# Kernel optimization log

Hardware: AMD Instinct MI355X
Metric: run time of the kernel (lower is better)

Reference implementation:

```python
import jax, jax.numpy as jnp
import numpy as np

KROT = 8        # number of pairwise-rotation layers (hard-coded in Rotation)
GROUP = 128     # rotation group size (hard-coded)
QGS = 128       # quantization group size (hard-coded in RotateLinearAWQMarlinInt4)


def setup_inputs() -> dict:
    rng = np.random.default_rng(0)
    M, K, N = 32, 8192, 28672
    G = K // QGS  # 64 quant groups
    shifts = np.arange(8, dtype=np.uint32) * 4
    # activations
    x = jnp.asarray(rng.standard_normal((M, K)), dtype=jnp.float16)
    # int4 weights packed 8-per-int32 along the out dim (nibble j of word n -> column n*8+j)
    nib = rng.integers(0, 16, size=(K, N // 8, 8), dtype=np.uint32)
    qweight = jnp.asarray((nib << shifts).sum(-1, dtype=np.uint32).view(np.int32))  # (K, N//8)
    znib = rng.integers(0, 16, size=(G, N // 8, 8), dtype=np.uint32)
    qzeros = jnp.asarray((znib << shifts).sum(-1, dtype=np.uint32).view(np.int32))  # (G, N//8)
    scales = jnp.asarray(rng.uniform(0.001, 0.01, (G, N)), dtype=jnp.float16)
    bias = jnp.asarray(rng.standard_normal(N) * 0.01, dtype=jnp.float16)
    # rotation params: per-layer angles over all K//2 pairs; one local permutation of
    # 0..127 per layer, shared across all K//GROUP groups (as in Rotation.__init__)
    theta = jnp.asarray(rng.uniform(-0.2, 0.2, (KROT, K // 2)), dtype=jnp.float16)
    pairs = jnp.asarray(np.stack([rng.permutation(GROUP) for _ in range(KROT)]).astype(np.int32))  # (KROT, 128)
    channel_scales = jnp.asarray(rng.uniform(0.5, 2.0, (1, K)), dtype=jnp.float16)
    return dict(x=x, qweight=qweight, qzeros=qzeros, scales=scales, bias=bias,
                theta=theta, pairs=pairs, channel_scales=channel_scales)


def _rotate(x, pairs, theta, channel_scales):
    # x: (M, K). Apply KROT layers of Givens rotations on channel pairs within each
    # 128-wide group, then per-channel scaling.
    M, K = x.shape
    ng = K // GROUP
    xg = x.reshape(M, ng, GROUP)
    for k in range(KROT):
        p = pairs[k]                      # (128,) local permutation
        i, j = p[0::2], p[1::2]           # (64,) disjoint index sets
        th = theta[k].reshape(ng, GROUP // 2).astype(jnp.float32)  # (ng, 64) per-group angles
        c = jnp.cos(th).astype(x.dtype)
        s = jnp.sin(th).astype(x.dtype)
        xi = xg[:, :, i]
        xj = xg[:, :, j]
        xg = xg.at[:, :, i].set(c * xi - s * xj)
        xg = xg.at[:, :, j].set(s * xi + c * xj)
    return xg.reshape(M, K) * channel_scales


def _dequant(qweight, qzeros, scales):
    # unpack 8 uint4 nibbles per int32 along the out dim; dequant per quant group
    K = qweight.shape[0]
    shifts = jnp.arange(8, dtype=jnp.int32) * 4
    w = ((qweight[:, :, None] >> shifts) & 0xF).reshape(K, -1)       # (K, N) ints 0..15
    z = ((qzeros[:, :, None] >> shifts) & 0xF).reshape(qzeros.shape[0], -1)  # (G, N)
    zf = jnp.repeat(z.astype(scales.dtype), QGS, axis=0)             # (K, N)
    sf = jnp.repeat(scales, QGS, axis=0)                             # (K, N)
    return (w.astype(scales.dtype) - zf) * sf


def reference(x, qweight, qzeros, scales, bias, theta, pairs, channel_scales):
    xr = _rotate(x, pairs, theta, channel_scales)   # (M, K)
    W = _dequant(qweight, qzeros, scales)           # (K, N)
    return xr @ W + bias
```

## Files before the change

kernel.cpp:

```cpp
#include <hip/hip_runtime.h>
#include <hip/hip_bf16.h>

using uint32   = unsigned int;
using ushort_t = unsigned short;
using short8   = __attribute__((ext_vector_type(8))) short;
using uint4v   = __attribute__((ext_vector_type(4))) uint32;
using float4v  = __attribute__((ext_vector_type(4))) float;
using floatx16 = __attribute__((ext_vector_type(16))) float;

#define M_DIM 32
#define K_DIM 8192
#define N_DIM 28672
#define QROW  (N_DIM/8)
#define KSPLIT 16
#define BN    256
#define CH    128
#define NCH   4
#define TSTRIDE 132

__device__ ushort_t g_xr2[M_DIM * K_DIM];
__device__ float    g_S[64 * M_DIM];

__device__ __forceinline__ float bf2f(ushort_t u){
  unsigned int v = ((unsigned int)u) << 16;
  return __builtin_bit_cast(float, v);
}
__device__ __forceinline__ ushort_t f2bf(float f){
  return __builtin_bit_cast(ushort_t, __float2bfloat16(f));
}

__global__ __launch_bounds__(256) void rotate_kernel(
    const float* __restrict__ x, const float* __restrict__ theta,
    const int* __restrict__ pairs, const float* __restrict__ cs)
{
  __shared__ float xb[4][128];
  const int u    = threadIdx.x >> 6;
  const int lane = threadIdx.x & 63;
  const int id   = blockIdx.x * 4 + u;
  const int m    = id >> 6;
  const int g    = id & 63;
  const float* xp = x + m*K_DIM + g*128;
  int   ip[8], jp[8];
  float cv[8], sv[8];
  #pragma unroll
  for (int k = 0; k < 8; ++k){
    ip[k] = pairs[k*128 + 2*lane];
    jp[k] = pairs[k*128 + 2*lane + 1];
    const float th = theta[k*(K_DIM/2) + g*64 + lane];
    cv[k] = cosf(th); sv[k] = sinf(th);
  }
  xb[u][lane]    = xp[lane];
  xb[u][lane+64] = xp[lane+64];
  #pragma unroll
  for (int k = 0; k < 8; ++k){
    __syncthreads();
    const float xi = xb[u][ip[k]], xj = xb[u][jp[k]];
    xb[u][ip[k]] = cv[k]*xi - sv[k]*xj;
    xb[u][jp[k]] = sv[k]*xi + cv[k]*xj;
  }
  __syncthreads();
  const int base = g*128;
  const int k0 = base + lane, k1 = base + lane + 64;
  const ushort_t b0 = f2bf(xb[u][lane]    * cs[k0]);
  const ushort_t b1 = f2bf(xb[u][lane+64] * cs[k1]);
  g_xr2[(((size_t)(k0>>3))*32 + m)*8 + (k0&7)] = b0;
  g_xr2[(((size_t)(k1>>3))*32 + m)*8 + (k1&7)] = b1;
  float sum = bf2f(b0) + bf2f(b1);
  #pragma unroll
  for (int d = 32; d > 0; d >>= 1) sum += __shfl_xor(sum, d, 64);
  if (lane == 0) g_S[g*M_DIM + m] = sum;
}

__global__ __launch_bounds__(256) void bias_kernel(
    const float* __restrict__ bias, float* __restrict__ out)
{
  const int n  = (blockIdx.x % (N_DIM/256))*256 + threadIdx.x;
  const int m0 = (blockIdx.x / (N_DIM/256))*8;
  const float b = bias[n];
  #pragma unroll
  for (int m = 0; m < 8; ++m) out[(size_t)(m0+m)*N_DIM + n] = b;
}

__global__ __launch_bounds__(512, 4) void gemm_kernel(
    const uint32* __restrict__ qw, const uint32* __restrict__ qz,
    const float* __restrict__ scales, float* __restrict__ out)
{
  __shared__ uint32 T[2][32*TSTRIDE];
  const int bid  = blockIdx.x;
  const int ks   = bid & (KSPLIT-1);
  const int nb   = bid >> 4;
  const int tid  = threadIdx.x;
  const int w    = tid >> 6;
  const int lane = tid & 63;
  const int l31  = lane & 31;
  const int koct = lane >> 5;
  const int n0   = nb * BN;
  const int n    = n0 + w*32 + l31;
  const uint32 sh = (uint32)((l31 & 7)*4);
  const int col  = w*4 + (l31 >> 3);
  const int k0   = ks * (NCH*CH);

  const int brow = tid >> 3;
  const int bcq  = tid & 7;
  const uint32* bbase = qw + (size_t)(k0 + brow)*QROW + (n0>>3) + bcq*4;
  const ushort_t* abase = g_xr2 + (size_t)k0*32;

  float accT[16];
  #pragma unroll
  for (int r = 0; r < 16; ++r) accT[r] = 0.f;

  uint4v bv0[2], bv1[2];

  bv0[0] = *(const uint4v*)(bbase);
  bv1[0] = *(const uint4v*)(bbase + (size_t)64*QROW);
  #pragma unroll
  for (int j = 0; j < 4; ++j){
    T[0][(bcq*4 + j)*TSTRIDE + brow]      = bv0[0][j];
    T[0][(bcq*4 + j)*TSTRIDE + brow + 64] = bv1[0][j];
  }
  bv0[1] = *(const uint4v*)(bbase + (size_t)CH*QROW);
  bv1[1] = *(const uint4v*)(bbase + (size_t)CH*QROW + (size_t)64*QROW);
  __syncthreads();

  #pragma unroll
  for (int c = 0; c < NCH; ++c){
    const int cb = c & 1, nx = cb ^ 1;
    if (c + 2 < NCH){
      const uint32* bb = bbase + (size_t)(c+2)*CH*QROW;
      bv0[cb] = *(const uint4v*)(bb);
      bv1[cb] = *(const uint4v*)(bb + (size_t)64*QROW);
    }
    if (c + 1 < NCH){
      #pragma unroll
      for (int j = 0; j < 4; ++j){
        T[nx][(bcq*4 + j)*TSTRIDE + brow]      = bv0[nx][j];
        T[nx][(bcq*4 + j)*TSTRIDE + brow + 64] = bv1[nx][j];
      }
    }

    const float  s  = scales[(size_t)(ks*NCH + c)*N_DIM + n];
    const uint32 zq = qz[(size_t)(ks*NCH + c)*QROW + (n>>3)];
    const ushort_t* ab = abase + (size_t)c*CH*32;

    floatx16 acc;
    #pragma unroll
    for (int r = 0; r < 16; ++r) acc[r] = 0.f;

    #pragma unroll
    for (int kh = 0; kh < 2; ++kh){
      short8 av[4];
      #pragma unroll
      for (int i = 0; i < 4; ++i){
        const int kk = kh*4 + i;
        av[i] = *(const short8*)(ab + ((kk*2 + koct)*32 + l31)*8);
      }
      #pragma unroll
      for (int i = 0; i < 4; ++i){
        const int kk = kh*4 + i;
        const uint32* tp = &T[cb][col*TSTRIDE + kk*16 + koct*8];
        const uint4v p0 = *(const uint4v*)(tp);
        const uint4v p1 = *(const uint4v*)(tp + 4);
        uint4v bp;
        bp.x = ((p0.x >> sh) & 15u) | (((p0.y >> sh) & 15u) << 16) | 0x43004300u;
        bp.y = ((p0.z >> sh) & 15u) | (((p0.w >> sh) & 15u) << 16) | 0x43004300u;
        bp.z = ((p1.x >> sh) & 15u) | (((p1.y >> sh) & 15u) << 16) | 0x43004300u;
        bp.w = ((p1.z >> sh) & 15u) | (((p1.w >> sh) & 15u) << 16) | 0x43004300u;
        acc = __builtin_amdgcn_mfma_f32_32x32x16_bf16(
                  av[i], __builtin_bit_cast(short8, bp), acc, 0, 0, 0);
      }
    }
    const float t = s * (float)(128u + ((zq >> sh) & 15u));
    const float* Sg = &g_S[(size_t)(ks*NCH + c)*M_DIM];
    float4v Sv[4];
    #pragma unroll
    for (int q = 0; q < 4; ++q)
      Sv[q] = *(const float4v*)(Sg + q*8 + 4*koct);
    #pragma unroll
    for (int r = 0; r < 16; ++r){
      accT[r] = fmaf(s, acc[r], accT[r]);
      accT[r] = fmaf(-t, Sv[r >> 2][r & 3], accT[r]);
    }
    if (c + 1 < NCH) __syncthreads();
  }
  #pragma unroll
  for (int r = 0; r < 16; ++r){
    const int row = (r & 3) + 8*(r >> 2) + 4*koct;
    atomicAdd(out + (size_t)row*N_DIM + n, accT[r]);
  }
}

extern "C" void kernel_launch(void* const* d_in, const int* in_sizes, int n_in,
                              void* d_out, int out_size, void* d_ws, size_t ws_size,
                              hipStream_t stream)
{
  const float*  x      = (const float*)d_in[0];
  const uint32* qw     = (const uint32*)d_in[1];
  const uint32* qz     = (const uint32*)d_in[2];
  const float*  scales = (const float*)d_in[3];
  const float*  bias   = (const float*)d_in[4];
  const float*  theta  = (const float*)d_in[5];
  const int*    pairs  = (const int*)d_in[6];
  const float*  cs     = (const float*)d_in[7];
  float* out = (float*)d_out;

  rotate_kernel<<<dim3((M_DIM*64)/4), dim3(256), 0, stream>>>(x, theta, pairs, cs);
  bias_kernel<<<dim3((N_DIM/256)*4), dim3(256), 0, stream>>>(bias, out);
  gemm_kernel<<<dim3((N_DIM/BN)*KSPLIT), dim3(512), 0, stream>>>(qw, qz, scales, out);
}
```

Baseline: 231.5 us.

## Fuse rotate and bias kernels, hoist scale loads, swizzle LDS stores, custom barrier

The rotation and bias-initialisation kernels are merged into one launch, with extra blocks handling the bias fill, which removes one kernel launch. The GEMM kernel now loads all per-chunk scales and zeros up front and rotates the order of its LDS transpose stores to spread bank conflicts. It replaces __syncthreads with a barrier that waits only on LDS counters, and asks for 8 blocks per CU in launch bounds. The higher occupancy target may limit registers and cause spills.

```diff
diff --git a/kernel.cpp b/kernel.cpp
--- a/kernel.cpp
+++ b/kernel.cpp
@@ -29,10 +29,26 @@
   return __builtin_bit_cast(ushort_t, __float2bfloat16(f));
 }
 
-__global__ __launch_bounds__(256) void rotate_kernel(
+#define LDS_BARRIER() do {                                   \
+  asm volatile("s_waitcnt lgkmcnt(0)" ::: "memory");         \
+  __builtin_amdgcn_s_barrier();                              \
+  asm volatile("" ::: "memory");                             \
+} while (0)
+
+__global__ __launch_bounds__(256) void prep_kernel(
     const float* __restrict__ x, const float* __restrict__ theta,
-    const int* __restrict__ pairs, const float* __restrict__ cs)
+    const int* __restrict__ pairs, const float* __restrict__ cs,
+    const float* __restrict__ bias, float* __restrict__ out)
 {
+  if (blockIdx.x >= 512){
+    const int b  = blockIdx.x - 512;
+    const int n  = (b % (N_DIM/256))*256 + threadIdx.x;
+    const int m0 = (b / (N_DIM/256))*8;
+    const float bv = bias[n];
+    #pragma unroll
+    for (int m = 0; m < 8; ++m) out[(size_t)(m0+m)*N_DIM + n] = bv;
+    return;
+  }
   __shared__ float xb[4][128];
   const int u    = threadIdx.x >> 6;
   const int lane = threadIdx.x & 63;
@@ -71,17 +87,7 @@
   if (lane == 0) g_S[g*M_DIM + m] = sum;
 }
 
-__global__ __launch_bounds__(256) void bias_kernel(
-    const float* __restrict__ bias, float* __restrict__ out)
-{
-  const int n  = (blockIdx.x % (N_DIM/256))*256 + threadIdx.x;
-  const int m0 = (blockIdx.x / (N_DIM/256))*8;
-  const float b = bias[n];
-  #pragma unroll
-  for (int m = 0; m < 8; ++m) out[(size_t)(m0+m)*N_DIM + n] = b;
-}
-
-__global__ __launch_bounds__(512, 4) void gemm_kernel(
+__global__ __launch_bounds__(512, 8) void gemm_kernel(
     const uint32* __restrict__ qw, const uint32* __restrict__ qz,
     const float* __restrict__ scales, float* __restrict__ out)
 {
@@ -105,6 +111,14 @@
   const uint32* bbase = qw + (size_t)(k0 + brow)*QROW + (n0>>3) + bcq*4;
   const ushort_t* abase = g_xr2 + (size_t)k0*32;
 
+  float  sc[NCH];
+  uint32 zc[NCH];
+  #pragma unroll
+  for (int c = 0; c < NCH; ++c){
+    sc[c] = scales[(size_t)(ks*NCH + c)*N_DIM + n];
+    zc[c] = qz[(size_t)(ks*NCH + c)*QROW + (n>>3)];
+  }
+
   float accT[16];
   #pragma unroll
   for (int r = 0; r < 16; ++r) accT[r] = 0.f;
@@ -115,12 +129,13 @@
   bv1[0] = *(const uint4v*)(bbase + (size_t)64*QROW);
   #pragma unroll
   for (int j = 0; j < 4; ++j){
-    T[0][(bcq*4 + j)*TSTRIDE + brow]      = bv0[0][j];
-    T[0][(bcq*4 + j)*TSTRIDE + brow + 64] = bv1[0][j];
+    const int mj = (j + bcq) & 3;
+    T[0][(bcq*4 + mj)*TSTRIDE + brow]      = bv0[0][mj];
+    T[0][(bcq*4 + mj)*TSTRIDE + brow + 64] = bv1[0][mj];
   }
   bv0[1] = *(const uint4v*)(bbase + (size_t)CH*QROW);
   bv1[1] = *(const uint4v*)(bbase + (size_t)CH*QROW + (size_t)64*QROW);
-  __syncthreads();
+  LDS_BARRIER();
 
   #pragma unroll
   for (int c = 0; c < NCH; ++c){
@@ -133,13 +148,12 @@
     if (c + 1 < NCH){
       #pragma unroll
       for (int j = 0; j < 4; ++j){
-        T[nx][(bcq*4 + j)*TSTRIDE + brow]      = bv0[nx][j];
-        T[nx][(bcq*4 + j)*TSTRIDE + brow + 64] = bv1[nx][j];
+        const int mj = (j + bcq) & 3;
+        T[nx][(bcq*4 + mj)*TSTRIDE + brow]      = bv0[nx][mj];
+        T[nx][(bcq*4 + mj)*TSTRIDE + brow + 64] = bv1[nx][mj];
       }
     }
 
-    const float  s  = scales[(size_t)(ks*NCH + c)*N_DIM + n];
-    const uint32 zq = qz[(size_t)(ks*NCH + c)*QROW + (n>>3)];
     const ushort_t* ab = abase + (size_t)c*CH*32;
 
     floatx16 acc;
@@ -169,7 +183,7 @@
                   av[i], __builtin_bit_cast(short8, bp), acc, 0, 0, 0);
       }
     }
-    const float t = s * (float)(128u + ((zq >> sh) & 15u));
+    const float t = sc[c] * (float)(128u + ((zc[c] >> sh) & 15u));
     const float* Sg = &g_S[(size_t)(ks*NCH + c)*M_DIM];
     float4v Sv[4];
     #pragma unroll
@@ -177,10 +191,10 @@
       Sv[q] = *(const float4v*)(Sg + q*8 + 4*koct);
     #pragma unroll
     for (int r = 0; r < 16; ++r){
-      accT[r] = fmaf(s, acc[r], accT[r]);
+      accT[r] = fmaf(sc[c], acc[r], accT[r]);
       accT[r] = fmaf(-t, Sv[r >> 2][r & 3], accT[r]);
     }
-    if (c + 1 < NCH) __syncthreads();
+    if (c + 1 < NCH) LDS_BARRIER();
   }
   #pragma unroll
   for (int r = 0; r < 16; ++r){
@@ -203,7 +217,7 @@
   const float*  cs     = (const float*)d_in[7];
   float* out = (float*)d_out;
 
-  rotate_kernel<<<dim3((M_DIM*64)/4), dim3(256), 0, stream>>>(x, theta, pairs, cs);
-  bias_kernel<<<dim3((N_DIM/256)*4), dim3(256), 0, stream>>>(bias, out);
+  prep_kernel<<<dim3(512 + (N_DIM/256)*4), dim3(256), 0, stream>>>(
+      x, theta, pairs, cs, bias, out);
   gemm_kernel<<<dim3((N_DIM/BN)*KSPLIT), dim3(512), 0, stream>>>(qw, qz, scales, out);
 }
```

Measured after the change: 279.0 us. 1.2x slower.
